# Kernel tuning notes

Hardware: AMD Instinct MI355X
Metric: run time of the kernel (lower is better)

## Reference

```python
import jax, jax.numpy as jnp
import numpy as np

TEMPERATURE = 0.1
SIGMA = 1.0
NUM_CLASSES = 4
INF = 1e8
EPS = 1e-12


def _l2_normalize(x):
    n = jnp.sqrt(jnp.sum(x * x, axis=-1, keepdims=True))
    return x / jnp.maximum(n, EPS)


def _rbf_kernel(y, gamma):
    # y: [M, P] -> [M, M] exp(-gamma * ||yi - yj||^2)
    sq = jnp.sum(y * y, axis=-1)
    d2 = sq[:, None] + sq[None, :] - 2.0 * (y @ y.T)
    d2 = jnp.maximum(d2, 0.0)
    return jnp.exp(-gamma * d2)


def setup_inputs() -> dict:
    key = jax.random.key(0)
    k1, k2, k3, k4 = jax.random.split(key, 4)
    N, D = 2048, 512
    return {
        "z_i": jax.random.normal(k1, (N, D), dtype=jnp.float32),
        "z_j": jax.random.normal(k2, (N, D), dtype=jnp.float32),
        "labels": jax.random.randint(k3, (N,), 0, NUM_CLASSES, dtype=jnp.int64),
        "z_pos": jax.random.uniform(k4, (N, 1), dtype=jnp.float32),
    }


def reference(z_i, z_j, labels, z_pos):
    N = z_i.shape[0]
    zi = _l2_normalize(z_i)
    zj = _l2_normalize(z_j)

    eye_n = jnp.eye(N, dtype=zi.dtype)
    sim_zii = (zi @ zi.T) / TEMPERATURE - INF * eye_n
    sim_zjj = (zj @ zj.T) / TEMPERATURE - INF * eye_n
    sim_zij = (zi @ zj.T) / TEMPERATURE

    # label agreement mask over the 2N x 2N augmented batch
    labs = jax.nn.one_hot(labels, NUM_CLASSES, dtype=jnp.float32)
    L = jnp.concatenate([labs, labs], axis=0)          # [2N, C]
    eye_2n = jnp.eye(2 * N, dtype=jnp.float32)
    mask = (L @ L.T) * (1.0 - eye_2n)

    # RBF kernel weights over positional labels (detached in original)
    all_pos = jnp.tile(z_pos.reshape(N, -1), (2, 1))   # [2N, P]
    gamma = 1.0 / (2.0 * SIGMA ** 2)
    weights = _rbf_kernel(all_pos, gamma) * (1.0 - eye_2n)

    final_weights = weights * mask
    # NB: torch broadcasting divides column j by rowsum[j]; matrix is symmetric
    final_weights = final_weights / final_weights.sum(axis=1)

    top = jnp.concatenate([sim_zii, sim_zij], axis=1)
    bot = jnp.concatenate([sim_zij.T, sim_zjj], axis=1)
    sim_Z = jnp.concatenate([top, bot], axis=0)        # [2N, 2N]

    log_sim_Z = jax.nn.log_softmax(sim_Z, axis=1)
    loss = (-1.0 / N) * jnp.sum(log_sim_Z * final_weights)
    return loss
```

## Files before the change

kernel.cpp:

```cpp
#include <hip/hip_runtime.h>
#include <hip/hip_bf16.h>

#define D 512
#define INV_T 10.0f
#define INF_VAL 1e8f

#define BM 128
#define BK 64
#define KSTEPS (D / BK)
#define NTB 32
#define NBLK (NTB * (NTB + 1) / 2)
#define TTBLK 128
#define NCHUNK 64

typedef short bf16x8 __attribute__((ext_vector_type(8)));
typedef float f32x4 __attribute__((ext_vector_type(4)));

typedef __attribute__((address_space(3))) unsigned int lds_uint;
typedef __attribute__((address_space(1))) unsigned int gbl_uint;

__device__ __forceinline__ void async_copy16(const ushort* gsrc, ushort* ldst) {
  __builtin_amdgcn_global_load_lds((const gbl_uint*)gsrc, (lds_uint*)ldst, 16, 0, 0);
}

__device__ inline float wave_reduce_sum(float v) {
#pragma unroll
  for (int off = 32; off > 0; off >>= 1) v += __shfl_xor(v, off);
  return v;
}

__device__ __forceinline__ ushort f2bf(float x) {
  __hip_bfloat16 h = __float2bfloat16(x);
  return *reinterpret_cast<ushort*>(&h);
}

__global__ __launch_bounds__(256) void k_prep(const float* __restrict__ zi,
                                              const float* __restrict__ zj,
                                              ushort* __restrict__ zb,
                                              const int* __restrict__ labels,
                                              const float* __restrict__ zpos,
                                              float* __restrict__ sinv, int N) {
  int b = blockIdx.x;
  if (b < 1024) {
    int wv = threadIdx.x >> 6, lane = threadIdx.x & 63;
    int row = b * 4 + wv;
    const float* src = (row < N) ? (zi + (size_t)row * D) : (zj + (size_t)(row - N) * D);
    const float4* s4 = reinterpret_cast<const float4*>(src);
    float4 v0 = s4[lane];
    float4 v1 = s4[lane + 64];
    float ss = 0.f;
    ss = fmaf(v0.x, v0.x, ss); ss = fmaf(v0.y, v0.y, ss);
    ss = fmaf(v0.z, v0.z, ss); ss = fmaf(v0.w, v0.w, ss);
    ss = fmaf(v1.x, v1.x, ss); ss = fmaf(v1.y, v1.y, ss);
    ss = fmaf(v1.z, v1.z, ss); ss = fmaf(v1.w, v1.w, ss);
    ss = wave_reduce_sum(ss);
    float sc = 1.0f / fmaxf(sqrtf(ss), 1e-12f);
    ushort4 o0 = {f2bf(v0.x * sc), f2bf(v0.y * sc), f2bf(v0.z * sc), f2bf(v0.w * sc)};
    ushort4 o1 = {f2bf(v1.x * sc), f2bf(v1.y * sc), f2bf(v1.z * sc), f2bf(v1.w * sc)};
    ushort4* dst = reinterpret_cast<ushort4*>(zb + (size_t)row * D);
    dst[lane] = o0;
    dst[lane + 64] = o1;
  } else {
    __shared__ float scratch[4];
    int j = b - 1024;
    int lj = labels[j];
    float pj = zpos[j];
    float s = 0.f;
    for (int i = threadIdx.x; i < N; i += 256) {
      if (labels[i] == lj) {
        float d = zpos[i] - pj;
        s += __expf(-0.5f * d * d);
      }
    }
    s = wave_reduce_sum(s);
    int lane = threadIdx.x & 63, wv = threadIdx.x >> 6;
    if (lane == 0) scratch[wv] = s;
    __syncthreads();
    if (threadIdx.x == 0) {
      float t = scratch[0] + scratch[1] + scratch[2] + scratch[3];
      sinv[j] = 1.0f / (2.0f * t - 1.0f);
    }
  }
}

__global__ __launch_bounds__(256, 2) void k_gemm(
    const ushort* __restrict__ zb, const int* __restrict__ labels,
    const float* __restrict__ zpos, const float* __restrict__ sinv,
    float* __restrict__ tt,
    float* __restrict__ s_ws, float* __restrict__ c_ws, int N) {
  const int tid = threadIdx.x;
  const int bid = blockIdx.x;
  const int twoN = 2 * N;

  if (bid >= NBLK) {
    int i = (bid - NBLK) * 16 + (tid >> 4);
    int part = tid & 15;
    int li = labels[i];
    float pi = zpos[i];
    int seg = N >> 4;
    float s = 0.f;
    for (int j = part * seg; j < (part + 1) * seg; ++j) {
      if (labels[j] == li) {
        float d = zpos[j] - pi;
        s += __expf(-0.5f * d * d) * sinv[j];
      }
    }
    s += __shfl_xor(s, 1); s += __shfl_xor(s, 2);
    s += __shfl_xor(s, 4); s += __shfl_xor(s, 8);
    if (part == 0) tt[i] = s;
    return;
  }

  __shared__ __align__(16) ushort sT[2][2][BM * BK];

  const int lane = tid & 63;
  const int wv = tid >> 6;
  const int wr = wv >> 1;
  const int wc = wv & 1;
  const int colq = lane & 15;
  const int laneg = lane >> 4;

  int L = (bid & 7) * (NBLK / 8) + (bid >> 3);
  int u = L, rt = 0;
  while (u >= NTB - rt) { u -= NTB - rt; ++rt; }
  const int ct = rt + u;
  const bool diag = (rt == ct);
  const int rowBase = rt * BM;
  const int colBase = ct * BM;

  const int srow = lane >> 3;
  const int sslot = (lane & 7) ^ srow;

  f32x4 acc[4][4] = {};

#pragma unroll
  for (int q = 0; q < 4; ++q) {
    int rloc = wv * 32 + q * 8;
    async_copy16(zb + (size_t)(rowBase + rloc + srow) * D + 0 * BK + sslot * 8,
                 (ushort*)sT[0][0] + rloc * BK);
    if (!diag)
      async_copy16(zb + (size_t)(colBase + rloc + srow) * D + 0 * BK + sslot * 8,
                   (ushort*)sT[0][1] + rloc * BK);
  }
  __syncthreads();

  int cur = 0;
#pragma unroll
  for (int kt = 0; kt < KSTEPS; ++kt) {
    if (kt + 1 < KSTEPS) {
#pragma unroll
      for (int q = 0; q < 4; ++q) {
        int rloc = wv * 32 + q * 8;
        async_copy16(zb + (size_t)(rowBase + rloc + srow) * D + (kt + 1) * BK + sslot * 8,
                     (ushort*)sT[cur ^ 1][0] + rloc * BK);
        if (!diag)
          async_copy16(zb + (size_t)(colBase + rloc + srow) * D + (kt + 1) * BK + sslot * 8,
                       (ushort*)sT[cur ^ 1][1] + rloc * BK);
      }
    }

    const char* Ab = reinterpret_cast<const char*>(sT[cur][0]);
    const char* Bb = diag ? Ab : reinterpret_cast<const char*>(sT[cur][1]);
#pragma unroll
    for (int kk = 0; kk < 2; ++kk) {
      bf16x8 a[4], b[4];
      const int slot = kk * 4 + laneg;
#pragma unroll
      for (int rf = 0; rf < 4; ++rf) {
        int r = wr * 64 + rf * 16 + colq;
        a[rf] = *reinterpret_cast<const bf16x8*>(Ab + r * 128 + (slot ^ (r & 7)) * 16);
      }
#pragma unroll
      for (int cf = 0; cf < 4; ++cf) {
        int c = wc * 64 + cf * 16 + colq;
        b[cf] = *reinterpret_cast<const bf16x8*>(Bb + c * 128 + (slot ^ (c & 7)) * 16);
      }
#pragma unroll
      for (int rf = 0; rf < 4; ++rf)
#pragma unroll
        for (int cf = 0; cf < 4; ++cf)
          acc[rf][cf] = __builtin_amdgcn_mfma_f32_16x16x32_bf16(a[rf], b[cf], acc[rf][cf], 0, 0, 0);
    }

    if (kt + 1 < KSTEPS) {
      __syncthreads();
      cur ^= 1;
    }
  }

  const int wRowBase = rowBase + wr * 64;
  const int wColBase = colBase + wc * 64;
  const int rmodBase = (wRowBase >= N) ? wRowBase - N : wRowBase;
  const int cmodBase = (wColBase >= N) ? wColBase - N : wColBase;

  float rpos[16], rsinv[16];
  unsigned rlab = 0;
#pragma unroll
  for (int rf = 0; rf < 4; ++rf)
#pragma unroll
    for (int rg = 0; rg < 4; ++rg) {
      int idx = rf * 4 + rg;
      int r = rmodBase + rf * 16 + laneg * 4 + rg;
      rpos[idx] = zpos[r];
      rsinv[idx] = sinv[r];
      rlab |= ((unsigned)labels[r] & 3u) << (idx * 2);
    }

  float s_p[16], c_p[16], sc_p[4], cc_p[4];
#pragma unroll
  for (int i = 0; i < 16; ++i) { s_p[i] = 0.f; c_p[i] = 0.f; }

#pragma unroll
  for (int cf = 0; cf < 4; ++cf) {
    int jc = cmodBase + cf * 16 + colq;
    int lc = labels[jc];
    float pc = zpos[jc];
    float si = sinv[jc];
    int col = wColBase + cf * 16 + colq;
    float scf = 0.f, ccf = 0.f;
#pragma unroll
    for (int rf = 0; rf < 4; ++rf)
#pragma unroll
      for (int rg = 0; rg < 4; ++rg) {
        int idx = rf * 4 + rg;
        int row = wRowBase + rf * 16 + laneg * 4 + rg;
        float sim = acc[rf][cf][rg] * INV_T;
        bool dg = (row == col);
        if (dg) sim = -INF_VAL;
        float e = __expf(sim - 10.f);
        s_p[idx] += e;
        scf += e;
        int lr = (int)((rlab >> (idx * 2)) & 3u);
        if (lr == lc && !dg) {
          float d = rpos[idx] - pc;
          float w = __expf(-0.5f * d * d);
          c_p[idx] = fmaf(w * si, sim, c_p[idx]);
          ccf = fmaf(w * rsinv[idx], sim, ccf);
        }
      }
    sc_p[cf] = scf;
    cc_p[cf] = ccf;
  }

#pragma unroll
  for (int idx = 0; idx < 16; ++idx) {
#pragma unroll
    for (int off = 1; off < 16; off <<= 1) {
      s_p[idx] += __shfl_xor(s_p[idx], off);
      c_p[idx] += __shfl_xor(c_p[idx], off);
    }
  }
  if (colq == 0) {
    int m = ct * 2 + wc;
#pragma unroll
    for (int rf = 0; rf < 4; ++rf)
#pragma unroll
      for (int rg = 0; rg < 4; ++rg) {
        int idx = rf * 4 + rg;
        int row = wRowBase + rf * 16 + laneg * 4 + rg;
        s_ws[(size_t)m * twoN + row] = s_p[idx];
        c_ws[(size_t)m * twoN + row] = c_p[idx];
      }
  }

  if (!diag) {
#pragma unroll
    for (int cf = 0; cf < 4; ++cf) {
      sc_p[cf] += __shfl_xor(sc_p[cf], 16);
      sc_p[cf] += __shfl_xor(sc_p[cf], 32);
      cc_p[cf] += __shfl_xor(cc_p[cf], 16);
      cc_p[cf] += __shfl_xor(cc_p[cf], 32);
    }
    if (laneg == 0) {
      int m = rt * 2 + wr;
#pragma unroll
      for (int cf = 0; cf < 4; ++cf) {
        int rowt = wColBase + cf * 16 + colq;
        s_ws[(size_t)m * twoN + rowt] = sc_p[cf];
        c_ws[(size_t)m * twoN + rowt] = cc_p[cf];
      }
    }
  }
}

__global__ __launch_bounds__(256) void k_combine(const float* __restrict__ s_ws,
                                                 const float* __restrict__ c_ws,
                                                 const float* __restrict__ sinv,
                                                 const float* __restrict__ tt,
                                                 float* __restrict__ bsum, int N) {
  __shared__ float sS[4][64], sC[4][64];
  int b = blockIdx.x, t = threadIdx.x;
  int r = t & 63, g = t >> 6;
  int twoN = 2 * N;
  int a = b * 64 + r;
  float s = 0.f, c = 0.f;
  for (int k = 0; k < NCHUNK / 4; ++k) {
    int m = g * (NCHUNK / 4) + k;
    s += s_ws[(size_t)m * twoN + a];
    c += c_ws[(size_t)m * twoN + a];
  }
  sS[g][r] = s;
  sC[g][r] = c;
  __syncthreads();
  if (t < 64) {
    float st = sS[0][t] + sS[1][t] + sS[2][t] + sS[3][t];
    float ct = sC[0][t] + sC[1][t] + sC[2][t] + sC[3][t];
    int aa = b * 64 + t;
    int ir = (aa >= N) ? aa - N : aa;
    float lse = 10.f + logf(st);
    float wsum = 2.f * tt[ir] - sinv[ir];
    float p = ct - wsum * lse;
    p = wave_reduce_sum(p);
    if (t == 0) bsum[b] = p;
  }
}

__global__ __launch_bounds__(64) void k_final(const float* __restrict__ bsum,
                                              float* __restrict__ out, int N) {
  float s = bsum[threadIdx.x];
  s = wave_reduce_sum(s);
  if (threadIdx.x == 0) out[0] = (-1.0f / (float)N) * s;
}

extern "C" void kernel_launch(void* const* d_in, const int* in_sizes, int n_in,
                              void* d_out, int out_size, void* d_ws, size_t ws_size,
                              hipStream_t stream) {
  (void)n_in; (void)out_size; (void)ws_size;
  const float* zi = (const float*)d_in[0];
  const float* zj = (const float*)d_in[1];
  const int* labels = (const int*)d_in[2];
  const float* zpos = (const float*)d_in[3];
  float* out = (float*)d_out;

  const int N = in_sizes[2];
  const int twoN = 2 * N;

  char* wsb = (char*)d_ws;
  ushort* zb = (ushort*)wsb;
  float* sinv = (float*)(wsb + (size_t)twoN * D * 2);
  float* tt = sinv + N;
  float* s_ws = tt + N;
  float* c_ws = s_ws + (size_t)NCHUNK * twoN;
  float* bsum = c_ws + (size_t)NCHUNK * twoN;

  k_prep<<<1024 + 2048, 256, 0, stream>>>(zi, zj, zb, labels, zpos, sinv, N);
  k_gemm<<<NBLK + TTBLK, 256, 0, stream>>>(zb, labels, zpos, sinv, tt, s_ws, c_ws, N);
  k_combine<<<twoN / 64, 256, 0, stream>>>(s_ws, c_ws, sinv, tt, bsum, N);
  k_final<<<1, 64, 0, stream>>>(bsum, out, N);
}
```

Measured before the change: 60.14 us.

## Replace symmetric 128-tile GEMM with full-grid 256-tile GEMM

Drops the upper-triangular symmetric tiling, where each 128x128 tile also produced transposed column partials, in favour of a full 16x16 grid of 256x256 tiles. Each tile uses 512 threads, 8 waves with 128x64 per wave, and BK=32. The change is meant to raise per-block arithmetic intensity and simplify the epilogue by removing the transposed reduction and its writes. The cost is computing every off-diagonal similarity twice and more accumulator register pressure. The tt side blocks now handle 32 rows each and are placed first in the grid.

```diff
diff --git a/kernel.cpp b/kernel.cpp
--- a/kernel.cpp
+++ b/kernel.cpp
@@ -5,12 +5,12 @@
 #define INV_T 10.0f
 #define INF_VAL 1e8f
 
-#define BM 128
-#define BK 64
+#define TILE 256
+#define BK 32
 #define KSTEPS (D / BK)
-#define NTB 32
-#define NBLK (NTB * (NTB + 1) / 2)
-#define TTBLK 128
+#define NGT 16
+#define NGB (NGT * NGT)
+#define TTB 64
 #define NCHUNK 64
 
 typedef short bf16x8 __attribute__((ext_vector_type(8)));
@@ -83,7 +83,7 @@
   }
 }
 
-__global__ __launch_bounds__(256, 2) void k_gemm(
+__global__ __launch_bounds__(512, 2) void k_main(
     const ushort* __restrict__ zb, const int* __restrict__ labels,
     const float* __restrict__ zpos, const float* __restrict__ sinv,
     float* __restrict__ tt,
@@ -92,8 +92,8 @@
   const int bid = blockIdx.x;
   const int twoN = 2 * N;
 
-  if (bid >= NBLK) {
-    int i = (bid - NBLK) * 16 + (tid >> 4);
+  if (bid < TTB) {
+    int i = bid * 32 + (tid >> 4);
     int part = tid & 15;
     int li = labels[i];
     float pi = zpos[i];
@@ -111,173 +111,134 @@
     return;
   }
 
-  __shared__ __align__(16) ushort sT[2][2][BM * BK];
+  __shared__ __align__(16) ushort As[2][TILE * BK];
+  __shared__ __align__(16) ushort Bs[2][TILE * BK];
 
   const int lane = tid & 63;
   const int wv = tid >> 6;
-  const int wr = wv >> 1;
-  const int wc = wv & 1;
+  const int wr = wv >> 2;
+  const int wc = wv & 3;
   const int colq = lane & 15;
   const int laneg = lane >> 4;
 
-  int L = (bid & 7) * (NBLK / 8) + (bid >> 3);
-  int u = L, rt = 0;
-  while (u >= NTB - rt) { u -= NTB - rt; ++rt; }
-  const int ct = rt + u;
-  const bool diag = (rt == ct);
-  const int rowBase = rt * BM;
-  const int colBase = ct * BM;
-
-  const int srow = lane >> 3;
-  const int sslot = (lane & 7) ^ srow;
-
-  f32x4 acc[4][4] = {};
-
-#pragma unroll
-  for (int q = 0; q < 4; ++q) {
-    int rloc = wv * 32 + q * 8;
-    async_copy16(zb + (size_t)(rowBase + rloc + srow) * D + 0 * BK + sslot * 8,
-                 (ushort*)sT[0][0] + rloc * BK);
-    if (!diag)
-      async_copy16(zb + (size_t)(colBase + rloc + srow) * D + 0 * BK + sslot * 8,
-                   (ushort*)sT[0][1] + rloc * BK);
-  }
+  int b = bid - TTB;
+  int L = (b & 7) * 32 + (b >> 3);
+  const int rt = L >> 4;
+  const int ct = L & 15;
+  const int rowBase = rt * TILE;
+  const int colBase = ct * TILE;
+
+  const int srow = lane >> 2;
+  const int sslot = (lane & 3) ^ ((lane >> 3) & 3);
+
+  f32x4 acc[8][4] = {};
+
+#define STAGE(buf, kt)                                                        \
+  {                                                                           \
+    _Pragma("unroll")                                                         \
+    for (int q = 0; q < 2; ++q) {                                             \
+      int r0 = wv * 32 + q * 16;                                              \
+      async_copy16(zb + (size_t)(rowBase + r0 + srow) * D + (kt) * BK +       \
+                       sslot * 8,                                             \
+                   As[buf] + r0 * BK);                                        \
+      async_copy16(zb + (size_t)(colBase + r0 + srow) * D + (kt) * BK +       \
+                       sslot * 8,                                             \
+                   Bs[buf] + r0 * BK);                                        \
+    }                                                                         \
+  }
+
+  STAGE(0, 0);
   __syncthreads();
 
   int cur = 0;
 #pragma unroll
   for (int kt = 0; kt < KSTEPS; ++kt) {
-    if (kt + 1 < KSTEPS) {
-#pragma unroll
-      for (int q = 0; q < 4; ++q) {
-        int rloc = wv * 32 + q * 8;
-        async_copy16(zb + (size_t)(rowBase + rloc + srow) * D + (kt + 1) * BK + sslot * 8,
-                     (ushort*)sT[cur ^ 1][0] + rloc * BK);
-        if (!diag)
-          async_copy16(zb + (size_t)(colBase + rloc + srow) * D + (kt + 1) * BK + sslot * 8,
-                       (ushort*)sT[cur ^ 1][1] + rloc * BK);
-      }
-    }
-
-    const char* Ab = reinterpret_cast<const char*>(sT[cur][0]);
-    const char* Bb = diag ? Ab : reinterpret_cast<const char*>(sT[cur][1]);
-#pragma unroll
-    for (int kk = 0; kk < 2; ++kk) {
-      bf16x8 a[4], b[4];
-      const int slot = kk * 4 + laneg;
-#pragma unroll
-      for (int rf = 0; rf < 4; ++rf) {
-        int r = wr * 64 + rf * 16 + colq;
-        a[rf] = *reinterpret_cast<const bf16x8*>(Ab + r * 128 + (slot ^ (r & 7)) * 16);
-      }
-#pragma unroll
-      for (int cf = 0; cf < 4; ++cf) {
-        int c = wc * 64 + cf * 16 + colq;
-        b[cf] = *reinterpret_cast<const bf16x8*>(Bb + c * 128 + (slot ^ (c & 7)) * 16);
-      }
-#pragma unroll
-      for (int rf = 0; rf < 4; ++rf)
-#pragma unroll
-        for (int cf = 0; cf < 4; ++cf)
-          acc[rf][cf] = __builtin_amdgcn_mfma_f32_16x16x32_bf16(a[rf], b[cf], acc[rf][cf], 0, 0, 0);
-    }
+    if (kt + 1 < KSTEPS) STAGE(cur ^ 1, kt + 1);
+
+    const char* Ab = reinterpret_cast<const char*>(As[cur]);
+    const char* Bb = reinterpret_cast<const char*>(Bs[cur]);
+    bf16x8 a[8], bf[4];
+#pragma unroll
+    for (int rf = 0; rf < 8; ++rf) {
+      int r = wr * 128 + rf * 16 + colq;
+      a[rf] = *reinterpret_cast<const bf16x8*>(
+          Ab + r * 64 + ((laneg ^ ((r >> 1) & 3)) << 4));
+    }
+#pragma unroll
+    for (int cf = 0; cf < 4; ++cf) {
+      int c = wc * 64 + cf * 16 + colq;
+      bf[cf] = *reinterpret_cast<const bf16x8*>(
+          Bb + c * 64 + ((laneg ^ ((c >> 1) & 3)) << 4));
+    }
+#pragma unroll
+    for (int rf = 0; rf < 8; ++rf)
+#pragma unroll
+      for (int cf = 0; cf < 4; ++cf)
+        acc[rf][cf] = __builtin_amdgcn_mfma_f32_16x16x32_bf16(a[rf], bf[cf], acc[rf][cf], 0, 0, 0);
 
     if (kt + 1 < KSTEPS) {
       __syncthreads();
       cur ^= 1;
     }
   }
-
-  const int wRowBase = rowBase + wr * 64;
+#undef STAGE
+
+  const int wRowBase = rowBase + wr * 128;
   const int wColBase = colBase + wc * 64;
   const int rmodBase = (wRowBase >= N) ? wRowBase - N : wRowBase;
   const int cmodBase = (wColBase >= N) ? wColBase - N : wColBase;
 
-  float rpos[16], rsinv[16];
-  unsigned rlab = 0;
-#pragma unroll
-  for (int rf = 0; rf < 4; ++rf)
-#pragma unroll
-    for (int rg = 0; rg < 4; ++rg) {
-      int idx = rf * 4 + rg;
-      int r = rmodBase + rf * 16 + laneg * 4 + rg;
-      rpos[idx] = zpos[r];
-      rsinv[idx] = sinv[r];
-      rlab |= ((unsigned)labels[r] & 3u) << (idx * 2);
-    }
-
-  float s_p[16], c_p[16], sc_p[4], cc_p[4];
-#pragma unroll
-  for (int i = 0; i < 16; ++i) { s_p[i] = 0.f; c_p[i] = 0.f; }
-
+  int lc[4]; float pc[4], si[4];
 #pragma unroll
   for (int cf = 0; cf < 4; ++cf) {
     int jc = cmodBase + cf * 16 + colq;
-    int lc = labels[jc];
-    float pc = zpos[jc];
-    float si = sinv[jc];
-    int col = wColBase + cf * 16 + colq;
-    float scf = 0.f, ccf = 0.f;
-#pragma unroll
-    for (int rf = 0; rf < 4; ++rf)
+    lc[cf] = labels[jc];
+    pc[cf] = zpos[jc];
+    si[cf] = sinv[jc];
+  }
+  const int m = ct * 4 + wc;
+
+#pragma unroll
+  for (int rf = 0; rf < 8; ++rf) {
+    float rpos[4]; int rlab[4];
+#pragma unroll
+    for (int rg = 0; rg < 4; ++rg) {
+      int r = rmodBase + rf * 16 + laneg * 4 + rg;
+      rpos[rg] = zpos[r];
+      rlab[rg] = labels[r];
+    }
+    float s_p[4] = {0.f, 0.f, 0.f, 0.f};
+    float c_p[4] = {0.f, 0.f, 0.f, 0.f};
+#pragma unroll
+    for (int cf = 0; cf < 4; ++cf) {
+      int col = wColBase + cf * 16 + colq;
 #pragma unroll
       for (int rg = 0; rg < 4; ++rg) {
-        int idx = rf * 4 + rg;
         int row = wRowBase + rf * 16 + laneg * 4 + rg;
         float sim = acc[rf][cf][rg] * INV_T;
         bool dg = (row == col);
         if (dg) sim = -INF_VAL;
-        float e = __expf(sim - 10.f);
-        s_p[idx] += e;
-        scf += e;
-        int lr = (int)((rlab >> (idx * 2)) & 3u);
-        if (lr == lc && !dg) {
-          float d = rpos[idx] - pc;
-          float w = __expf(-0.5f * d * d);
-          c_p[idx] = fmaf(w * si, sim, c_p[idx]);
-          ccf = fmaf(w * rsinv[idx], sim, ccf);
+        s_p[rg] += __expf(sim - 10.f);
+        if (rlab[rg] == lc[cf] && !dg) {
+          float d = rpos[rg] - pc[cf];
+          c_p[rg] = fmaf(__expf(-0.5f * d * d) * si[cf], sim, c_p[rg]);
         }
       }
-    sc_p[cf] = scf;
-    cc_p[cf] = ccf;
-  }
-
-#pragma unroll
-  for (int idx = 0; idx < 16; ++idx) {
-#pragma unroll
-    for (int off = 1; off < 16; off <<= 1) {
-      s_p[idx] += __shfl_xor(s_p[idx], off);
-      c_p[idx] += __shfl_xor(c_p[idx], off);
-    }
-  }
-  if (colq == 0) {
-    int m = ct * 2 + wc;
-#pragma unroll
-    for (int rf = 0; rf < 4; ++rf)
+    }
+#pragma unroll
+    for (int rg = 0; rg < 4; ++rg) {
+#pragma unroll
+      for (int off = 1; off < 16; off <<= 1) {
+        s_p[rg] += __shfl_xor(s_p[rg], off);
+        c_p[rg] += __shfl_xor(c_p[rg], off);
+      }
+    }
+    if (colq == 0) {
 #pragma unroll
       for (int rg = 0; rg < 4; ++rg) {
-        int idx = rf * 4 + rg;
         int row = wRowBase + rf * 16 + laneg * 4 + rg;
-        s_ws[(size_t)m * twoN + row] = s_p[idx];
-        c_ws[(size_t)m * twoN + row] = c_p[idx];
-      }
-  }
-
-  if (!diag) {
-#pragma unroll
-    for (int cf = 0; cf < 4; ++cf) {
-      sc_p[cf] += __shfl_xor(sc_p[cf], 16);
-      sc_p[cf] += __shfl_xor(sc_p[cf], 32);
-      cc_p[cf] += __shfl_xor(cc_p[cf], 16);
-      cc_p[cf] += __shfl_xor(cc_p[cf], 32);
-    }
-    if (laneg == 0) {
-      int m = rt * 2 + wr;
-#pragma unroll
-      for (int cf = 0; cf < 4; ++cf) {
-        int rowt = wColBase + cf * 16 + colq;
-        s_ws[(size_t)m * twoN + rowt] = sc_p[cf];
-        c_ws[(size_t)m * twoN + rowt] = cc_p[cf];
+        s_ws[(size_t)m * twoN + row] = s_p[rg];
+        c_ws[(size_t)m * twoN + row] = c_p[rg];
       }
     }
   }
@@ -344,7 +305,7 @@
   float* bsum = c_ws + (size_t)NCHUNK * twoN;
 
   k_prep<<<1024 + 2048, 256, 0, stream>>>(zi, zj, zb, labels, zpos, sinv, N);
-  k_gemm<<<NBLK + TTBLK, 256, 0, stream>>>(zb, labels, zpos, sinv, tt, s_ws, c_ws, N);
+  k_main<<<TTB + NGB, 512, 0, stream>>>(zb, labels, zpos, sinv, tt, s_ws, c_ws, N);
   k_combine<<<twoN / 64, 256, 0, stream>>>(s_ws, c_ws, sinv, tt, bsum, N);
   k_final<<<1, 64, 0, stream>>>(bsum, out, N);
 }
```

Measured after the change: 70.75 us. 17.6% more time.
